# Kernel tuning notes

Hardware: AMD Instinct MI355X
Metric: run time of the kernel (lower is better)

The kernel has to match this reference:

```python
import jax, jax.numpy as jnp
import numpy as np

N, H, R2, T, E, POS, L = 50000, 256, 460, 3, 100000, 3, 2
RRELU_SLOPE = (1.0 / 8 + 1.0 / 3) / 2  # eval-mode rrelu = leaky with mean slope


def setup_inputs() -> dict:
    key = jax.random.key(0)
    ks = jax.random.split(key, 24)
    s = 0.05
    return {
        'src': jax.random.randint(ks[0], (T, E), 0, N, dtype=jnp.int32),
        'dst': jax.random.randint(ks[1], (T, E), 0, N, dtype=jnp.int32),
        'etype': jax.random.randint(ks[2], (T, E), 0, R2, dtype=jnp.int32),
        'r_to_e': jax.random.randint(ks[3], (T, E), 0, N, dtype=jnp.int32),
        'r_seg': jax.random.randint(ks[4], (T, E), 0, R2, dtype=jnp.int32),
        'pos_enc': jax.random.normal(ks[5], (T, N, POS), jnp.float32),
        'dynamic_emb': jax.random.normal(ks[6], (N, H), jnp.float32),
        'emb_rel': jax.random.normal(ks[7], (R2, H), jnp.float32) * s,
        'gru_W_ih': jax.random.normal(ks[8], (3 * H, 2 * H), jnp.float32) * s,
        'gru_W_hh': jax.random.normal(ks[9], (3 * H, H), jnp.float32) * s,
        'gru_b_ih': jnp.zeros((3 * H,), jnp.float32),
        'gru_b_hh': jnp.zeros((3 * H,), jnp.float32),
        'W_neigh': jax.random.normal(ks[10], (L, H, H), jnp.float32) * s,
        'W_loop': jax.random.normal(ks[11], (L, H, H), jnp.float32) * s,
        'W_evolve': jax.random.normal(ks[12], (L, H, H), jnp.float32) * s,
        'W_hp': jax.random.normal(ks[13], (H, H + POS), jnp.float32) * s,
        'b_hp': jnp.zeros((H,), jnp.float32),
        'W_v': jax.random.normal(ks[14], (H, H), jnp.float32) * s,
        'b_v': jnp.zeros((H,), jnp.float32),
        'W_o': jax.random.normal(ks[15], (H, H), jnp.float32) * s,
        'b_o': jnp.zeros((H,), jnp.float32),
        'time_W': jax.random.normal(ks[16], (H, H), jnp.float32) * s,
        'time_b': jnp.zeros((H,), jnp.float32),
        'glob_W': jax.random.normal(ks[17], (H, H), jnp.float32) * s,
        'glob_b': jnp.zeros((H,), jnp.float32),
    }


def _l2norm(x):
    return x / jnp.maximum(jnp.linalg.norm(x, axis=-1, keepdims=True), 1e-12)


def _gru_cell(x, hprev, W_ih, W_hh, b_ih, b_hh):
    gi = x @ W_ih.T + b_ih
    gh = hprev @ W_hh.T + b_hh
    i_r, i_z, i_n = jnp.split(gi, 3, axis=-1)
    h_r, h_z, h_n = jnp.split(gh, 3, axis=-1)
    r = jax.nn.sigmoid(i_r + h_r)
    z = jax.nn.sigmoid(i_z + h_z)
    n = jnp.tanh(i_n + r * h_n)
    return (1.0 - z) * n + z * hprev


def _forward(src, dst, etype, r_to_e, r_seg, pos_enc, dynamic_emb, emb_rel,
             gru_W_ih, gru_W_hh, gru_b_ih, gru_b_hh,
             W_neigh, W_loop, W_evolve, W_hp, b_hp, W_v, b_v, W_o, b_o,
             time_W, time_b, glob_W, glob_b):
    h = _l2norm(dynamic_emb)  # layer_norm=True path: F.normalize
    h0 = emb_rel
    outs = []
    for t in range(T):  # sequence_len snapshots
        # per-relation mean of involved entity embeddings (r_len/uniq_r spans)
        feat = h[r_to_e[t]]                                   # [E, H]
        sums = jax.ops.segment_sum(feat, r_seg[t], num_segments=R2)
        cnts = jax.ops.segment_sum(jnp.ones((E,), feat.dtype), r_seg[t], num_segments=R2)
        x_mean = jnp.where(cnts[:, None] > 0, sums / jnp.maximum(cnts, 1.0)[:, None], 0.0)
        x_in = jnp.concatenate([emb_rel, x_mean], axis=1)     # [R2, 2H]
        h0 = _l2norm(_gru_cell(x_in, h0, gru_W_ih, gru_W_hh, gru_b_ih, gru_b_hh))
        # UnionRGCN layers: msg = (h_src + rel[etype]) @ W_neigh, sum-agg * 1/in_deg,
        # plus self-loop (loop_weight if in_deg>0 else evolve_loop_weight), rrelu.
        deg = jax.ops.segment_sum(jnp.ones((E,), h.dtype), dst[t], num_segments=N)
        norm = jnp.where(deg > 0, 1.0 / jnp.maximum(deg, 1.0), 0.0)[:, None]
        nh = h
        for l in range(L):
            msg = (nh[src[t]] + h0[etype[t]]) @ W_neigh[l]    # [E, H]
            agg = jax.ops.segment_sum(msg, dst[t], num_segments=N) * norm
            loop = jnp.where(deg[:, None] > 0, nh @ W_loop[l], nh @ W_evolve[l])
            pre = agg + loop
            nh = jnp.where(pre >= 0, pre, RRELU_SLOPE * pre)
        current_h = nh
        # global attention over seq-len-1 -> out_proj(v_proj(x)) in eval mode
        atten_in = jnp.tanh(jnp.concatenate([current_h, pos_enc[t]], axis=1) @ W_hp.T + b_hp)
        global_h = (atten_in @ W_v.T + b_v) @ W_o.T + b_o
        current_h = _l2norm(current_h)
        tw = jax.nn.sigmoid(h @ time_W + time_b)
        h = tw * current_h + (1.0 - tw) * h
        gw = jax.nn.sigmoid(h @ glob_W + glob_b)
        outs.append(gw * global_h + (1.0 - gw) * h)
    return jnp.stack(outs)  # [T, N, H] history_embs


def reference(src, dst, etype, r_to_e, r_seg, pos_enc, dynamic_emb, emb_rel,
              gru_W_ih, gru_W_hh, gru_b_ih, gru_b_hh,
              W_neigh, W_loop, W_evolve, W_hp, b_hp, W_v, b_v, W_o, b_o,
              time_W, time_b, glob_W, glob_b):
    return _forward(src, dst, etype, r_to_e, r_seg, pos_enc, dynamic_emb, emb_rel,
                    gru_W_ih, gru_W_hh, gru_b_ih, gru_b_hh,
                    W_neigh, W_loop, W_evolve, W_hp, b_hp, W_v, b_v, W_o, b_o,
                    time_W, time_b, glob_W, glob_b)
```

## Files before the change

kernel.cpp:

```cpp
#include <hip/hip_runtime.h>
#include <math.h>

#define NN 50000
#define HH 256
#define RR 460
#define TT 3
#define EE 100000
#define PP 3
#define SLOPE 0.22916666666666666f
#define NBIN (RR + NN)
#define NBIN3 (3*NBIN)

typedef __bf16 bf16_t;
typedef bf16_t bf16x8 __attribute__((ext_vector_type(8)));
typedef float f32x4 __attribute__((ext_vector_type(4)));

static const size_t NHf = (size_t)NN * HH;

__device__ __forceinline__ float sigm(float x){ return 1.0f/(1.0f+__expf(-x)); }
__device__ __forceinline__ float leaky(float x){ return (x >= 0.f) ? x : SLOPE*x; }

__device__ __forceinline__ void gload_lds16(const void* g, void* l){
  __builtin_amdgcn_global_load_lds((const __attribute__((address_space(1))) void*)g,
                                   (__attribute__((address_space(3))) void*)l, 16, 0, 0);
}

__global__ __launch_bounds__(256) void tconv_all_k(
    const float* __restrict__ Wn, const float* __restrict__ Wl, const float* __restrict__ We,
    const float* __restrict__ timW, const float* __restrict__ globW,
    bf16_t* __restrict__ bst2, bf16_t* __restrict__ wdT,
    bf16_t* __restrict__ timT, bf16_t* __restrict__ globT){
  int z = blockIdx.z;
  const float* in; const float* in2 = nullptr; bf16_t* outp; int ldout;
  switch(z){
    case 0: in = Wn;           outp = bst2;                       ldout = 512; break;
    case 1: in = Wl;           outp = bst2 + 256;                 ldout = 512; break;
    case 2: in = Wn + 65536;   outp = bst2 + (size_t)256*512;     ldout = 512; break;
    case 3: in = Wl + 65536;   outp = bst2 + (size_t)256*512+256; ldout = 512; break;
    case 4: in = We;          in2 = Wl;         outp = wdT;         ldout = 256; break;
    case 5: in = We + 65536;  in2 = Wl + 65536; outp = wdT + 65536; ldout = 256; break;
    case 6: in = timW;  outp = timT;  ldout = 256; break;
    default:in = globW; outp = globT; ldout = 256; break;
  }
  __shared__ float tile[32][33];
  int n0 = blockIdx.x*32, k0 = blockIdx.y*32;
  int tx = threadIdx.x & 31, ty = threadIdx.x >> 5;
  #pragma unroll
  for (int j=0;j<4;j++){
    size_t idx = (size_t)(k0+ty+j*8)*256 + n0+tx;
    float v = in[idx];
    if (in2) v -= in2[idx];
    tile[ty+j*8][tx] = v;
  }
  __syncthreads();
  #pragma unroll
  for (int j=0;j<4;j++)
    outp[(size_t)(n0+ty+j*8)*ldout + k0+tx] = (bf16_t)tile[tx][ty+j*8];
}

__global__ __launch_bounds__(256) void copyall_k(const float* __restrict__ gW_ih,
    const float* __restrict__ gW_hh, const float* __restrict__ W_hp, const float* __restrict__ emb_rel,
    bf16_t* __restrict__ wihAT, bf16_t* __restrict__ wihBT, bf16_t* __restrict__ whhT,
    bf16_t* __restrict__ whpT, bf16_t* __restrict__ h0b){
  int r = blockIdx.x, c = threadIdx.x, y = blockIdx.y;
  if (y == 0)      wihAT[(size_t)r*256+c] = (bf16_t)gW_ih[(size_t)r*512 + c];
  else if (y == 1) wihBT[(size_t)r*256+c] = (bf16_t)gW_ih[(size_t)r*512 + 256 + c];
  else if (y == 2) whhT[(size_t)r*256+c]  = (bf16_t)gW_hh[(size_t)r*256 + c];
  else if (y == 3){ if (r < 256) whpT[(size_t)r*256+c] = (bf16_t)W_hp[(size_t)r*259 + c]; }
  else            { if (r < RR)  h0b[(size_t)r*256+c]  = (bf16_t)emb_rel[(size_t)r*256 + c]; }
}

__global__ __launch_bounds__(256) void misc_k(const float* __restrict__ W_hp, float* __restrict__ WP,
    const float* __restrict__ W_o, const float* __restrict__ b_v, const float* __restrict__ b_o,
    float* __restrict__ b_ov){
  if (blockIdx.x == 0){
    int j = threadIdx.x;
    #pragma unroll
    for (int p=0;p<PP;p++) WP[p*HH + j] = W_hp[(size_t)j*259 + HH + p];
  } else {
    int n = threadIdx.x;
    float s = b_o[n];
    for (int j=0;j<256;j++) s += W_o[(size_t)n*256+j]*b_v[j];
    b_ov[n] = s;
  }
}

__global__ __launch_bounds__(256) void copy_bfw_k(const float* __restrict__ in, bf16_t* __restrict__ outp){
  int r = blockIdx.x, c = threadIdx.x;
  outp[(size_t)r*HH + c] = (bf16_t)in[(size_t)r*HH + c];
}

__global__ __launch_bounds__(256) void sgemm_k(const float* __restrict__ A, const float* __restrict__ B,
                                               float* __restrict__ C, int M, int N, int K){
  __shared__ float As[16][128];
  __shared__ float Bs[16][64];
  int tid = threadIdx.x;
  int tx = tid & 15, ty = tid >> 4;
  int rowBase = blockIdx.x * 128;
  int colBase = blockIdx.y * 64;
  float acc[8][4];
  #pragma unroll
  for (int i=0;i<8;i++)
    #pragma unroll
    for (int j=0;j<4;j++) acc[i][j]=0.f;
  for (int k0=0;k0<K;k0+=16){
    #pragma unroll
    for (int ss=0; ss<2; ss++){
      int s = tid + ss*256;
      int r = s >> 2;
      int kk = (s & 3)*4;
      float4 v = make_float4(0.f,0.f,0.f,0.f);
      int grow = rowBase + r;
      if (grow < M) v = *(const float4*)(A + (size_t)grow*K + k0 + kk);
      As[kk+0][r]=v.x; As[kk+1][r]=v.y; As[kk+2][r]=v.z; As[kk+3][r]=v.w;
    }
    {
      int r = tid >> 4, cc = (tid & 15)*4;
      float4 v = *(const float4*)(B + (size_t)(k0+r)*N + colBase + cc);
      *(float4*)&Bs[r][cc] = v;
    }
    __syncthreads();
    #pragma unroll
    for (int kk=0;kk<16;kk++){
      float a[8], b[4];
      *(float4*)&a[0] = *(const float4*)&As[kk][ty*8];
      *(float4*)&a[4] = *(const float4*)&As[kk][ty*8+4];
      *(float4*)&b[0] = *(const float4*)&Bs[kk][tx*4];
      #pragma unroll
      for (int i=0;i<8;i++)
        #pragma unroll
        for (int j=0;j<4;j++)
          acc[i][j] = fmaf(a[i], b[j], acc[i][j]);
    }
    __syncthreads();
  }
  #pragma unroll
  for (int i=0;i<8;i++){
    int gr = rowBase + ty*8 + i;
    if (gr >= M) continue;
    float4 v = make_float4(acc[i][0], acc[i][1], acc[i][2], acc[i][3]);
    *(float4*)(C + (size_t)gr*N + colBase + tx*4) = v;
  }
}

template<int EPI, int HASB>
__global__ __launch_bounds__(256) void mgemm_k(
    const bf16_t* __restrict__ A0, const bf16_t* __restrict__ Bt,
    float* __restrict__ C, const float* __restrict__ bias,
    int M, int N, int K, const float* __restrict__ e1){
  __shared__ bf16_t As[128*64];
  __shared__ bf16_t Bs[128*64];
  int tid = threadIdx.x;
  int lane = tid & 63, w = tid >> 6;
  int wm = w >> 1, wn = w & 1;
  int rowBase = blockIdx.x * 128;
  int colBase = blockIdx.y * 128;
  f32x4 acc[4][4] = {};

  int lrow = lane >> 3;
  int p    = lane & 7;
  int arow[4];
  #pragma unroll
  for (int c = 0; c < 4; c++){
    int gr = rowBase + c*32 + w*8 + lrow;
    arow[c] = min(gr, M-1);
  }
  for (int k0 = 0; k0 < K; k0 += 64){
    #pragma unroll
    for (int c = 0; c < 4; c++){
      int r = c*32 + w*8 + lrow;
      int s = p ^ (r & 7);
      gload_lds16(A0 + (size_t)arow[c]*K + k0 + s*8, As + (size_t)(c*32 + w*8)*64);
      int gb = colBase + r;
      gload_lds16(Bt + (size_t)gb*K + k0 + s*8, Bs + (size_t)(c*32 + w*8)*64);
    }
    asm volatile("s_waitcnt vmcnt(0)" ::: "memory");
    __syncthreads();
    #pragma unroll
    for (int kk = 0; kk < 2; kk++){
      bf16x8 af[4], bfr[4];
      int sg = kk*4 + (lane >> 4);
      #pragma unroll
      for (int i = 0; i < 4; i++){
        int r = wm*64 + i*16 + (lane & 15);
        af[i] = *(const bf16x8*)(As + r*64 + (sg ^ (r & 7))*8);
      }
      #pragma unroll
      for (int j = 0; j < 4; j++){
        int rn = wn*64 + j*16 + (lane & 15);
        bfr[j] = *(const bf16x8*)(Bs + rn*64 + (sg ^ (rn & 7))*8);
      }
      #pragma unroll
      for (int i = 0; i < 4; i++)
        #pragma unroll
        for (int j = 0; j < 4; j++)
          acc[i][j] = __builtin_amdgcn_mfma_f32_16x16x32_bf16(af[i], bfr[j], acc[i][j], 0, 0, 0);
    }
    __syncthreads();
  }
  int colv[4]; float bb[4];
  #pragma unroll
  for (int j = 0; j < 4; j++){
    colv[j] = colBase + wn*64 + j*16 + (lane & 15);
    bb[j] = HASB ? bias[colv[j]] : 0.f;
  }
  #pragma unroll
  for (int i = 0; i < 4; i++){
    #pragma unroll
    for (int q = 0; q < 4; q++){
      int grt = rowBase + wm*64 + i*16 + ((lane >> 4) << 2) + q;
      if (grt >= M) continue;
      #pragma unroll
      for (int j = 0; j < 4; j++){
        size_t idx = (size_t)grt*N + colv[j];
        float v = acc[i][j][q] + bb[j];
        if (EPI == 8) v += e1[idx];
        C[idx] = v;
      }
    }
  }
}

template<int EPI, int WF32, int WBF, int HASB, int SPLITA>
__global__ __launch_bounds__(512, 6) void mgemm2_k(
    const bf16_t* __restrict__ A0, const bf16_t* __restrict__ A1,
    const bf16_t* __restrict__ Bt,
    float* __restrict__ C, bf16_t* __restrict__ Cb, const float* __restrict__ bias,
    int M, int K,
    const float* __restrict__ e1, const float* __restrict__ e2,
    const bf16_t* __restrict__ eb, const bf16_t* __restrict__ eb2,
    const int* __restrict__ degp, const int* __restrict__ z, const int* __restrict__ nzp){
  int rowBase = blockIdx.x * 64;
  int nzv = 0;
  if (EPI == 5){
    nzv = nzp[0];
    if (rowBase >= nzv) return;
  }
  __shared__ bf16_t As[64*64];
  __shared__ bf16_t Bs[256*64];
  int tid = threadIdx.x;
  int lane = tid & 63, w = tid >> 6;
  f32x4 acc[4][2] = {};

  int lrow8 = lane >> 3;
  int p     = lane & 7;
  int arow;
  {
    int r = w*8 + lrow8;
    int gr = rowBase + r;
    if (EPI == 5) arow = z[min(gr, nzv-1)];
    else          arow = min(gr, M-1);
  }
  for (int k0 = 0; k0 < K; k0 += 64){
    const bf16_t* Ap; int koff; size_t lda;
    if (SPLITA){ Ap = (k0 < 256) ? A0 : A1; koff = k0 & 255; lda = 256; }
    else       { Ap = A0; koff = k0; lda = (size_t)K; }
    {
      int r = w*8 + lrow8;
      int s = p ^ (r & 7);
      gload_lds16(Ap + (size_t)arow*lda + koff + s*8, As + (size_t)(w*8)*64);
    }
    #pragma unroll
    for (int c = 0; c < 4; c++){
      int r = w*32 + c*8 + lrow8;
      int s = p ^ (r & 7);
      gload_lds16(Bt + (size_t)r*K + k0 + s*8, Bs + (size_t)(w*32 + c*8)*64);
    }
    asm volatile("s_waitcnt vmcnt(0)" ::: "memory");
    __syncthreads();
    #pragma unroll
    for (int kk = 0; kk < 2; kk++){
      bf16x8 af[4], bfr[2];
      int sg = kk*4 + (lane >> 4);
      #pragma unroll
      for (int i = 0; i < 4; i++){
        int r = i*16 + (lane & 15);
        af[i] = *(const bf16x8*)(As + r*64 + (sg ^ (r & 7))*8);
      }
      #pragma unroll
      for (int j = 0; j < 2; j++){
        int rn = w*32 + j*16 + (lane & 15);
        bfr[j] = *(const bf16x8*)(Bs + rn*64 + (sg ^ (rn & 7))*8);
      }
      #pragma unroll
      for (int i = 0; i < 4; i++)
        #pragma unroll
        for (int j = 0; j < 2; j++)
          acc[i][j] = __builtin_amdgcn_mfma_f32_16x16x32_bf16(af[i], bfr[j], acc[i][j], 0, 0, 0);
    }
    __syncthreads();
  }
  int colv[2]; float bb[2], wp0[2], wp1[2], wp2[2];
  #pragma unroll
  for (int j = 0; j < 2; j++){
    colv[j] = w*32 + j*16 + (lane & 15);
    bb[j] = HASB ? bias[colv[j]] : 0.f;
    if (EPI == 2){ wp0[j] = e2[colv[j]]; wp1[j] = e2[256+colv[j]]; wp2[j] = e2[512+colv[j]]; }
  }
  #pragma unroll
  for (int i = 0; i < 4; i++){
    #pragma unroll
    for (int q = 0; q < 4; q++){
      int grt = rowBase + i*16 + ((lane >> 4) << 2) + q;
      if (EPI == 5){ if (grt >= nzv) continue; }
      else         { if (grt >= M) continue; }
      int orow = (EPI == 5) ? z[grt] : grt;
      int dflag = 0;
      if (EPI == 4) dflag = degp[orow];
      float p0=0.f, p1=0.f, p2=0.f;
      if (EPI == 2){ p0 = e1[(size_t)grt*3]; p1 = e1[(size_t)grt*3+1]; p2 = e1[(size_t)grt*3+2]; }
      #pragma unroll
      for (int j = 0; j < 2; j++){
        size_t idx = (size_t)orow*256 + colv[j];
        float v = acc[i][j][q] + bb[j];
        if (EPI == 2) v = tanhf(v + p0*wp0[j] + p1*wp1[j] + p2*wp2[j]);
        if (EPI == 3){
          float g = sigm(v);
          v = g*(float)eb[idx] + (1.f-g)*(float)eb2[idx];
        }
        if (EPI == 4) v = (dflag > 0) ? leaky(v) : v;
        if (EPI == 5){
          float praw = (float)Cb[idx];
          v = leaky(praw + v);
        }
        if (EPI == 7) v = sigm(v);
        if (WF32) C[idx] = v;
        if (WBF)  Cb[idx] = (bf16_t)v;
      }
    }
  }
}

__global__ __launch_bounds__(256) void l2norm_k(const float* __restrict__ in, bf16_t* __restrict__ outb){
  int i = blockIdx.x, c = threadIdx.x;
  size_t idx = (size_t)i*HH + c;
  float v = in[idx];
  float ss = v*v;
  #pragma unroll
  for (int o=32;o;o>>=1) ss += __shfl_down(ss, o);
  __shared__ float red[4];
  if ((threadIdx.x & 63)==0) red[threadIdx.x>>6] = ss;
  __syncthreads();
  float tot = red[0]+red[1]+red[2]+red[3];
  outb[idx] = (bf16_t)(v / fmaxf(sqrtf(tot), 1e-12f));
}

__global__ __launch_bounds__(256) void hist3_k(const int* __restrict__ r_seg, const int* __restrict__ dst,
                                               int* __restrict__ cnt){
  int q = blockIdx.x*256 + threadIdx.x;
  if (q >= 3*2*EE) return;
  int t = q / (2*EE);
  int e = q - t*2*EE;
  if (e < EE) atomicAdd(cnt + t*NBIN + r_seg[(size_t)t*EE + e], 1);
  else        atomicAdd(cnt + t*NBIN + RR + dst[(size_t)t*EE + (e-EE)], 1);
}

__global__ __launch_bounds__(1024) void scan1_k(const int* __restrict__ cnt, int* __restrict__ start,
                                                int* __restrict__ bsum, int n){
  __shared__ int s[1024];
  int t = blockIdx.x*1024 + threadIdx.x;
  int v = (t < n) ? cnt[t] : 0;
  s[threadIdx.x] = v;
  __syncthreads();
  for (int off = 1; off < 1024; off <<= 1){
    int x = (threadIdx.x >= off) ? s[threadIdx.x - off] : 0;
    __syncthreads();
    s[threadIdx.x] += x;
    __syncthreads();
  }
  if (t < n) start[t] = s[threadIdx.x] - v;
  if (threadIdx.x == 1023) bsum[blockIdx.x] = s[1023];
}
__global__ __launch_bounds__(256) void scan2_k(const int* __restrict__ bsum, int* __restrict__ boff,
                                               int* __restrict__ start, int nb, int n){
  __shared__ int s[256];
  int t = threadIdx.x;
  int v = (t < nb) ? bsum[t] : 0;
  s[t] = v;
  __syncthreads();
  for (int off = 1; off < 256; off <<= 1){
    int x = (t >= off) ? s[t-off] : 0;
    __syncthreads();
    s[t] += x;
    __syncthreads();
  }
  if (t < nb) boff[t] = s[t] - v;
  if (t == 255) start[n] = s[255];
}
__global__ __launch_bounds__(1024) void scan3_k(int* __restrict__ start, int* __restrict__ cur,
                                                const int* __restrict__ boff, int n){
  int t = blockIdx.x*1024 + threadIdx.x;
  if (t < n){
    int v = start[t] + boff[blockIdx.x];
    start[t] = v;
    cur[t] = v;
  }
}

__global__ __launch_bounds__(256) void fill3_k(const int* __restrict__ r_seg, const int* __restrict__ r_to_e,
    const int* __restrict__ dst, const int* __restrict__ src, const int* __restrict__ ety,
    int* __restrict__ cur, int* __restrict__ rnode, unsigned* __restrict__ dpack){
  int q = blockIdx.x*256 + threadIdx.x;
  if (q >= 3*2*EE) return;
  int t = q / (2*EE);
  int e = q - t*2*EE;
  if (e < EE){
    size_t ge = (size_t)t*EE + e;
    int pp = atomicAdd(cur + t*NBIN + r_seg[ge], 1);
    rnode[pp - EE*t] = r_to_e[ge];
  } else {
    size_t ge = (size_t)t*EE + (e - EE);
    int pp = atomicAdd(cur + t*NBIN + RR + dst[ge], 1);
    dpack[pp - EE*(t+1)] = (unsigned)src[ge] | ((unsigned)ety[ge] << 16);
  }
}

__global__ __launch_bounds__(256) void compact3_k(const int* __restrict__ cnt, int* __restrict__ zAll,
                                                  int* __restrict__ nz){
  int q = blockIdx.x*256 + threadIdx.x;
  int lane = threadIdx.x & 63;
  bool valid = q < 3*NN;
  int qc = valid ? q : 3*NN - 1;
  int t = qc / NN, d = qc - t*NN;
  bool pred = valid && (cnt[t*NBIN + RR + d] == 0);
  int tA = __shfl(t, 0), tB = __shfl(t, 63);
  if (tA == tB){
    unsigned long long m = __ballot(pred);
    int total = __popcll(m);
    int base = 0;
    if (lane == 0 && total > 0) base = atomicAdd(nz + tA, total);
    base = __shfl(base, 0);
    if (pred){
      int myoff = __popcll(m & ((1ULL << lane) - 1ULL));
      zAll[(size_t)tA*NN + base + myoff] = d;
    }
  } else {
    if (pred){
      int pp = atomicAdd(nz + t, 1);
      zAll[(size_t)t*NN + pp] = d;
    }
  }
}

__global__ __launch_bounds__(256) void rmean_k(const int* __restrict__ startT, const int* __restrict__ rnode,
    const bf16_t* __restrict__ hb, bf16_t* __restrict__ meanb, int rbase){
  int r = blockIdx.x, c = threadIdx.x;
  int s0 = startT[r] - rbase, s1 = startT[r+1] - rbase;
  float acc = 0.f, acc2 = 0.f;
  int i = s0;
  for (; i + 1 < s1; i += 2){
    acc  += (float)hb[(size_t)rnode[i]*HH + c];
    acc2 += (float)hb[(size_t)rnode[i+1]*HH + c];
  }
  if (i < s1) acc += (float)hb[(size_t)rnode[i]*HH + c];
  acc += acc2;
  int cnt = s1 - s0;
  meanb[(size_t)r*HH + c] = (bf16_t)((cnt > 0) ? acc/(float)cnt : 0.f);
}

__global__ __launch_bounds__(256) void gru_gate_k(const float* __restrict__ gi,
    const float* __restrict__ ghb, float* __restrict__ h0, bf16_t* __restrict__ h0b){
  int r = blockIdx.x, c = threadIdx.x;
  float ir = gi[(size_t)r*768 + c],       hr = ghb[(size_t)r*768 + c];
  float iz = gi[(size_t)r*768 + 256 + c], hz = ghb[(size_t)r*768 + 256 + c];
  float in_ = gi[(size_t)r*768 + 512 + c], hn = ghb[(size_t)r*768 + 512 + c];
  float rg = sigm(ir + hr);
  float z  = sigm(iz + hz);
  float n  = tanhf(in_ + rg*hn);
  float hp = h0[(size_t)r*HH + c];
  float v = (1.f - z)*n + z*hp;
  float ss = v*v;
  #pragma unroll
  for (int o=32;o;o>>=1) ss += __shfl_down(ss, o);
  __shared__ float red[4];
  if ((threadIdx.x & 63)==0) red[threadIdx.x>>6] = ss;
  __syncthreads();
  float tot = red[0]+red[1]+red[2]+red[3];
  float nv = v / fmaxf(sqrtf(tot), 1e-12f);
  h0[(size_t)r*HH + c] = nv;
  h0b[(size_t)r*HH + c] = (bf16_t)nv;
}

__global__ __launch_bounds__(256) void gatherM_k(const bf16_t* __restrict__ nin,
    const bf16_t* __restrict__ h0b, const int* __restrict__ startT,
    const unsigned* __restrict__ dpack, bf16_t* __restrict__ Amean, int ebase){
  int w = threadIdx.x >> 6, ln = threadIdx.x & 63;
  int d = blockIdx.x*4 + w;
  if (d >= NN) return;
  int s0 = startT[RR + d] - ebase, s1 = startT[RR + d + 1] - ebase;
  int deg = s1 - s0;
  float a0=0.f, a1=0.f, a2=0.f, a3=0.f;
  int i = s0;
  for (; i + 1 < s1; i += 2){
    unsigned seA = dpack[i], seB = dpack[i+1];
    uint2 raA = *(const uint2*)(nin + (size_t)(seA & 0xffffu)*HH + ln*4);
    uint2 raB = *(const uint2*)(nin + (size_t)(seB & 0xffffu)*HH + ln*4);
    uint2 rbA = *(const uint2*)(h0b + (size_t)(seA >> 16)*HH + ln*4);
    uint2 rbB = *(const uint2*)(h0b + (size_t)(seB >> 16)*HH + ln*4);
    a0 += __uint_as_float((raA.x & 0xffffu) << 16) + __uint_as_float((rbA.x & 0xffffu) << 16)
        + __uint_as_float((raB.x & 0xffffu) << 16) + __uint_as_float((rbB.x & 0xffffu) << 16);
    a1 += __uint_as_float(raA.x & 0xffff0000u)     + __uint_as_float(rbA.x & 0xffff0000u)
        + __uint_as_float(raB.x & 0xffff0000u)     + __uint_as_float(rbB.x & 0xffff0000u);
    a2 += __uint_as_float((raA.y & 0xffffu) << 16) + __uint_as_float((rbA.y & 0xffffu) << 16)
        + __uint_as_float((raB.y & 0xffffu) << 16) + __uint_as_float((rbB.y & 0xffffu) << 16);
    a3 += __uint_as_float(raA.y & 0xffff0000u)     + __uint_as_float(rbA.y & 0xffff0000u)
        + __uint_as_float(raB.y & 0xffff0000u)     + __uint_as_float(rbB.y & 0xffff0000u);
  }
  if (i < s1){
    unsigned se = dpack[i];
    uint2 ra = *(const uint2*)(nin + (size_t)(se & 0xffffu)*HH + ln*4);
    uint2 rb = *(const uint2*)(h0b + (size_t)(se >> 16)*HH + ln*4);
    a0 += __uint_as_float((ra.x & 0xffffu) << 16) + __uint_as_float((rb.x & 0xffffu) << 16);
    a1 += __uint_as_float(ra.x & 0xffff0000u)     + __uint_as_float(rb.x & 0xffff0000u);
    a2 += __uint_as_float((ra.y & 0xffffu) << 16) + __uint_as_float((rb.y & 0xffffu) << 16);
    a3 += __uint_as_float(ra.y & 0xffff0000u)     + __uint_as_float(rb.y & 0xffff0000u);
  }
  float inv = (deg > 0) ? 1.f/(float)deg : 0.f;
  bf16_t m[4] = { (bf16_t)(a0*inv), (bf16_t)(a1*inv), (bf16_t)(a2*inv), (bf16_t)(a3*inv) };
  *(uint2*)(Amean + (size_t)d*HH + ln*4) = *(const uint2*)m;
}

__global__ __launch_bounds__(256) void l2up_k(const bf16_t* __restrict__ nh2b, const bf16_t* __restrict__ sg,
    bf16_t* __restrict__ hb){
  int i = blockIdx.x, c = threadIdx.x;
  size_t idx = (size_t)i*HH + c;
  float v = (float)nh2b[idx];
  float ss = v*v;
  #pragma unroll
  for (int o=32;o;o>>=1) ss += __shfl_down(ss, o);
  __shared__ float red[4];
  if ((threadIdx.x & 63)==0) red[threadIdx.x>>6] = ss;
  __syncthreads();
  float tot = red[0]+red[1]+red[2]+red[3];
  float curn = v / fmaxf(sqrtf(tot), 1e-12f);
  float s = (float)sg[idx];
  float hn = s*curn + (1.f-s)*(float)hb[idx];
  hb[idx] = (bf16_t)hn;
}

extern "C" void kernel_launch(void* const* d_in, const int* in_sizes, int n_in,
                              void* d_out, int out_size, void* d_ws, size_t ws_size,
                              hipStream_t stream) {
  const int*   src     = (const int*)  d_in[0];
  const int*   dst     = (const int*)  d_in[1];
  const int*   etype   = (const int*)  d_in[2];
  const int*   r_to_e  = (const int*)  d_in[3];
  const int*   r_seg   = (const int*)  d_in[4];
  const float* pos_enc = (const float*)d_in[5];
  const float* dyn_emb = (const float*)d_in[6];
  const float* emb_rel = (const float*)d_in[7];
  const float* gW_ih   = (const float*)d_in[8];
  const float* gW_hh   = (const float*)d_in[9];
  const float* gb_ih   = (const float*)d_in[10];
  const float* gb_hh   = (const float*)d_in[11];
  const float* W_neigh = (const float*)d_in[12];
  const float* W_loop  = (const float*)d_in[13];
  const float* W_evolve= (const float*)d_in[14];
  const float* W_hp    = (const float*)d_in[15];
  const float* b_hp    = (const float*)d_in[16];
  const float* W_v     = (const float*)d_in[17];
  const float* b_v     = (const float*)d_in[18];
  const float* W_o     = (const float*)d_in[19];
  const float* b_o     = (const float*)d_in[20];
  const float* time_W  = (const float*)d_in[21];
  const float* time_b  = (const float*)d_in[22];
  const float* glob_W  = (const float*)d_in[23];
  const float* glob_b  = (const float*)d_in[24];
  float* out = (float*)d_out;
  (void)in_sizes; (void)n_in; (void)out_size; (void)ws_size;

  char* ws = (char*)d_ws;
  size_t off = 0;
  auto allocB = [&](size_t bytes)->char*{
    char* pp = ws + off; off += (bytes + 255) & ~(size_t)255;
    return pp;
  };
  float*  tmp    = (float*) allocB(NHf*4);
  bf16_t* h_bf   = (bf16_t*)allocB(NHf*2);
  bf16_t* nh_bf  = (bf16_t*)allocB(NHf*2);
  bf16_t* nh2_bf = (bf16_t*)allocB(NHf*2);
  bf16_t* gh_bf  = (bf16_t*)allocB(NHf*2);
  bf16_t* Amean  = (bf16_t*)tmp;
  bf16_t* sgate  = (bf16_t*)(tmp + NHf/2);
  bf16_t* attn_bf= nh_bf;

  float*  h0    = (float*) allocB((size_t)RR*HH*4);
  bf16_t* h0b   = (bf16_t*)allocB((size_t)RR*HH*2);
  bf16_t* meanb = (bf16_t*)allocB((size_t)RR*HH*2);
  float*  gi0   = (float*) allocB((size_t)RR*768*4);
  float*  gi    = (float*) allocB((size_t)RR*768*4);
  float*  ghb   = (float*) allocB((size_t)RR*768*4);
  bf16_t* wihAT = (bf16_t*)allocB((size_t)768*256*2);
  bf16_t* wihBT = (bf16_t*)allocB((size_t)768*256*2);
  bf16_t* whhT  = (bf16_t*)allocB((size_t)768*256*2);
  float*  WP    = (float*) allocB((size_t)PP*HH*4);
  float*  WovF  = (float*) allocB((size_t)HH*HH*4);
  float*  b_ov  = (float*) allocB((size_t)HH*4);
  bf16_t* bst2  = (bf16_t*)allocB((size_t)2*HH*512*2);
  bf16_t* wdT   = (bf16_t*)allocB((size_t)2*HH*HH*2);
  bf16_t* whpT  = (bf16_t*)allocB((size_t)HH*HH*2);
  bf16_t* wovT  = (bf16_t*)allocB((size_t)HH*HH*2);
  bf16_t* timT  = (bf16_t*)allocB((size_t)HH*HH*2);
  bf16_t* globT = (bf16_t*)allocB((size_t)HH*HH*2);
  int* cnt    = (int*)allocB((size_t)(NBIN3+4)*4);
  int* start  = (int*)allocB((size_t)(NBIN3+1)*4);
  int* cur    = (int*)allocB((size_t)NBIN3*4);
  int* rnode  = (int*)allocB((size_t)3*EE*4);
  unsigned* dpack = (unsigned*)allocB((size_t)3*EE*4);
  int* zAll   = (int*)allocB((size_t)3*NN*4);
  int* bsum   = (int*)allocB(256*4);
  int* boff   = (int*)allocB(256*4);
  int* nz     = cnt + NBIN3;

  const int MT2 = (NN + 63)/64;
  const int NB3 = (NBIN3 + 1023)/1024;

  copyall_k<<<dim3(768,5), 256, 0, stream>>>(gW_ih, gW_hh, W_hp, emb_rel,
                                             wihAT, wihBT, whhT, whpT, h0b);
  tconv_all_k<<<dim3(8,8,8), 256, 0, stream>>>(W_neigh, W_loop, W_evolve, time_W, glob_W,
                                               bst2, wdT, timT, globT);
  misc_k<<<2, 256, 0, stream>>>(W_hp, WP, W_o, b_v, b_o, b_ov);
  sgemm_k<<<dim3(2,4), 256, 0, stream>>>(W_o, W_v, WovF, 256, 256, 256);
  copy_bfw_k<<<HH, 256, 0, stream>>>(WovF, wovT);
  l2norm_k<<<NN, 256, 0, stream>>>(dyn_emb, h_bf);
  hipMemcpyAsync(h0, emb_rel, (size_t)RR*HH*4, hipMemcpyDeviceToDevice, stream);
  mgemm_k<0,1><<<dim3(4,6), 256, 0, stream>>>(h0b, wihAT, gi0, gb_ih, RR, 768, 256, nullptr);

  hipMemsetAsync(cnt, 0, (size_t)(NBIN3+4)*4, stream);
  hist3_k<<<(6*EE+255)/256, 256, 0, stream>>>(r_seg, dst, cnt);
  scan1_k<<<NB3, 1024, 0, stream>>>(cnt, start, bsum, NBIN3);
  scan2_k<<<1, 256, 0, stream>>>(bsum, boff, start, NB3, NBIN3);
  scan3_k<<<NB3, 1024, 0, stream>>>(start, cur, boff, NBIN3);
  fill3_k<<<(6*EE+255)/256, 256, 0, stream>>>(r_seg, r_to_e, dst, src, etype, cur, rnode, dpack);
  compact3_k<<<(3*NN+255)/256, 256, 0, stream>>>(cnt, zAll, nz);

  for (int t=0; t<TT; t++){
    const float* posT = pos_enc + (size_t)t*NN*PP;
    const int* startT = start + (size_t)t*NBIN;
    const int* degT   = cnt + (size_t)t*NBIN + RR;
    const int* zT     = zAll + (size_t)t*NN;
    const int* nzT    = nz + t;

    rmean_k<<<RR, 256, 0, stream>>>(startT, rnode, h_bf, meanb, EE*t);
    mgemm_k<8,0><<<dim3(4,6), 256, 0, stream>>>(meanb, wihBT, gi, nullptr, RR, 768, 256, gi0);
    mgemm_k<0,1><<<dim3(4,6), 256, 0, stream>>>(h0b, whhT, ghb, gb_hh, RR, 768, 256, nullptr);
    gru_gate_k<<<RR, 256, 0, stream>>>(gi, ghb, h0, h0b);

    gatherM_k<<<(NN+3)/4, 256, 0, stream>>>(h_bf, h0b, startT, dpack, Amean, EE*(t+1));
    mgemm2_k<4,0,1,0,1><<<MT2, 512, 0, stream>>>(Amean, h_bf, bst2, nullptr, nh_bf, nullptr,
        NN, 512, nullptr, nullptr, nullptr, nullptr, degT, nullptr, nullptr);
    mgemm2_k<5,0,1,0,0><<<MT2, 512, 0, stream>>>(h_bf, nullptr, wdT, nullptr, nh_bf, nullptr,
        NN, 256, nullptr, nullptr, nullptr, nullptr, nullptr, zT, nzT);

    gatherM_k<<<(NN+3)/4, 256, 0, stream>>>(nh_bf, h0b, startT, dpack, Amean, EE*(t+1));
    mgemm2_k<4,0,1,0,1><<<MT2, 512, 0, stream>>>(Amean, nh_bf, bst2 + (size_t)HH*512, nullptr, nh2_bf, nullptr,
        NN, 512, nullptr, nullptr, nullptr, nullptr, degT, nullptr, nullptr);
    mgemm2_k<5,0,1,0,0><<<MT2, 512, 0, stream>>>(nh_bf, nullptr, wdT + (size_t)HH*HH, nullptr, nh2_bf, nullptr,
        NN, 256, nullptr, nullptr, nullptr, nullptr, nullptr, zT, nzT);

    mgemm2_k<2,0,1,1,0><<<MT2, 512, 0, stream>>>(nh2_bf, nullptr, whpT, nullptr, attn_bf, b_hp,
        NN, 256, posT, WP, nullptr, nullptr, nullptr, nullptr, nullptr);
    mgemm2_k<0,0,1,1,0><<<MT2, 512, 0, stream>>>(attn_bf, nullptr, wovT, nullptr, gh_bf, b_ov,
        NN, 256, nullptr, nullptr, nullptr, nullptr, nullptr, nullptr, nullptr);

    mgemm2_k<7,0,1,1,0><<<MT2, 512, 0, stream>>>(h_bf, nullptr, timT, nullptr, sgate, time_b,
        NN, 256, nullptr, nullptr, nullptr, nullptr, nullptr, nullptr, nullptr);
    l2up_k<<<NN, 256, 0, stream>>>(nh2_bf, sgate, h_bf);
    mgemm2_k<3,1,0,1,0><<<MT2, 512, 0, stream>>>(h_bf, nullptr, globT, out + (size_t)t*NHf, nullptr, glob_b,
        NN, 256, nullptr, nullptr, gh_bf, h_bf, nullptr, nullptr, nullptr);
  }
}
```

Measured before the change: 1.329 ms.

## Fuse zero-degree evolve correction into neighbor GEMM via third K-segment

Replaces the separate sparse evolve-correction GEMM (over compacted zero-in-degree nodes) with a third 256-wide K segment in the main neighbor/loop GEMM. Rows with degree zero load their own features there, and other rows load a zero row. Leaky activation is then applied uniformly in the epilogue. This removes the compaction kernel, one GEMM launch per layer and the read-modify-write of nh_bf. In exchange every row does 768-deep K work instead of 512 plus sparse extra work.

```diff
diff --git a/kernel.cpp b/kernel.cpp
--- a/kernel.cpp
+++ b/kernel.cpp
@@ -28,17 +28,16 @@
 __global__ __launch_bounds__(256) void tconv_all_k(
     const float* __restrict__ Wn, const float* __restrict__ Wl, const float* __restrict__ We,
     const float* __restrict__ timW, const float* __restrict__ globW,
-    bf16_t* __restrict__ bst2, bf16_t* __restrict__ wdT,
-    bf16_t* __restrict__ timT, bf16_t* __restrict__ globT){
+    bf16_t* __restrict__ bst3, bf16_t* __restrict__ timT, bf16_t* __restrict__ globT){
   int z = blockIdx.z;
   const float* in; const float* in2 = nullptr; bf16_t* outp; int ldout;
   switch(z){
-    case 0: in = Wn;           outp = bst2;                       ldout = 512; break;
-    case 1: in = Wl;           outp = bst2 + 256;                 ldout = 512; break;
-    case 2: in = Wn + 65536;   outp = bst2 + (size_t)256*512;     ldout = 512; break;
-    case 3: in = Wl + 65536;   outp = bst2 + (size_t)256*512+256; ldout = 512; break;
-    case 4: in = We;          in2 = Wl;         outp = wdT;         ldout = 256; break;
-    case 5: in = We + 65536;  in2 = Wl + 65536; outp = wdT + 65536; ldout = 256; break;
+    case 0: in = Wn;          outp = bst3;                          ldout = 768; break;
+    case 1: in = Wl;          outp = bst3 + 256;                    ldout = 768; break;
+    case 2: in = We;         in2 = Wl;         outp = bst3 + 512;   ldout = 768; break;
+    case 3: in = Wn + 65536;  outp = bst3 + (size_t)256*768;        ldout = 768; break;
+    case 4: in = Wl + 65536;  outp = bst3 + (size_t)256*768 + 256;  ldout = 768; break;
+    case 5: in = We + 65536; in2 = Wl + 65536; outp = bst3 + (size_t)256*768 + 512; ldout = 768; break;
     case 6: in = timW;  outp = timT;  ldout = 256; break;
     default:in = globW; outp = globT; ldout = 256; break;
   }
@@ -229,13 +228,8 @@
     int M, int K,
     const float* __restrict__ e1, const float* __restrict__ e2,
     const bf16_t* __restrict__ eb, const bf16_t* __restrict__ eb2,
-    const int* __restrict__ degp, const int* __restrict__ z, const int* __restrict__ nzp){
+    const int* __restrict__ degp, const bf16_t* __restrict__ zrow){
   int rowBase = blockIdx.x * 64;
-  int nzv = 0;
-  if (EPI == 5){
-    nzv = nzp[0];
-    if (rowBase >= nzv) return;
-  }
   __shared__ bf16_t As[64*64];
   __shared__ bf16_t Bs[256*64];
   int tid = threadIdx.x;
@@ -245,20 +239,26 @@
   int lrow8 = lane >> 3;
   int p     = lane & 7;
   int arow;
+  const bf16_t* a2base = nullptr;
   {
     int r = w*8 + lrow8;
-    int gr = rowBase + r;
-    if (EPI == 5) arow = z[min(gr, nzv-1)];
-    else          arow = min(gr, M-1);
+    arow = min(rowBase + r, M-1);
+    if (SPLITA == 2) a2base = (degp[arow] == 0) ? (A1 + (size_t)arow*256) : zrow;
   }
   for (int k0 = 0; k0 < K; k0 += 64){
-    const bf16_t* Ap; int koff; size_t lda;
-    if (SPLITA){ Ap = (k0 < 256) ? A0 : A1; koff = k0 & 255; lda = 256; }
-    else       { Ap = A0; koff = k0; lda = (size_t)K; }
+    const bf16_t* Ap; int koff;
+    if (SPLITA == 2){
+      Ap = (k0 < 256) ? (A0 + (size_t)arow*256)
+         : (k0 < 512) ? (A1 + (size_t)arow*256)
+         : a2base;
+      koff = k0 & 255;
+    } else {
+      Ap = A0 + (size_t)arow*K; koff = k0;
+    }
     {
       int r = w*8 + lrow8;
       int s = p ^ (r & 7);
-      gload_lds16(Ap + (size_t)arow*lda + koff + s*8, As + (size_t)(w*8)*64);
+      gload_lds16(Ap + koff + s*8, As + (size_t)(w*8)*64);
     }
     #pragma unroll
     for (int c = 0; c < 4; c++){
@@ -302,27 +302,19 @@
     #pragma unroll
     for (int q = 0; q < 4; q++){
       int grt = rowBase + i*16 + ((lane >> 4) << 2) + q;
-      if (EPI == 5){ if (grt >= nzv) continue; }
-      else         { if (grt >= M) continue; }
-      int orow = (EPI == 5) ? z[grt] : grt;
-      int dflag = 0;
-      if (EPI == 4) dflag = degp[orow];
+      if (grt >= M) continue;
       float p0=0.f, p1=0.f, p2=0.f;
       if (EPI == 2){ p0 = e1[(size_t)grt*3]; p1 = e1[(size_t)grt*3+1]; p2 = e1[(size_t)grt*3+2]; }
       #pragma unroll
       for (int j = 0; j < 2; j++){
-        size_t idx = (size_t)orow*256 + colv[j];
+        size_t idx = (size_t)grt*256 + colv[j];
         float v = acc[i][j][q] + bb[j];
         if (EPI == 2) v = tanhf(v + p0*wp0[j] + p1*wp1[j] + p2*wp2[j]);
         if (EPI == 3){
           float g = sigm(v);
           v = g*(float)eb[idx] + (1.f-g)*(float)eb2[idx];
         }
-        if (EPI == 4) v = (dflag > 0) ? leaky(v) : v;
-        if (EPI == 5){
-          float praw = (float)Cb[idx];
-          v = leaky(praw + v);
-        }
+        if (EPI == 6) v = leaky(v);
         if (EPI == 7) v = sigm(v);
         if (WF32) C[idx] = v;
         if (WBF)  Cb[idx] = (bf16_t)v;
@@ -412,33 +404,6 @@
     size_t ge = (size_t)t*EE + (e - EE);
     int pp = atomicAdd(cur + t*NBIN + RR + dst[ge], 1);
     dpack[pp - EE*(t+1)] = (unsigned)src[ge] | ((unsigned)ety[ge] << 16);
-  }
-}
-
-__global__ __launch_bounds__(256) void compact3_k(const int* __restrict__ cnt, int* __restrict__ zAll,
-                                                  int* __restrict__ nz){
-  int q = blockIdx.x*256 + threadIdx.x;
-  int lane = threadIdx.x & 63;
-  bool valid = q < 3*NN;
-  int qc = valid ? q : 3*NN - 1;
-  int t = qc / NN, d = qc - t*NN;
-  bool pred = valid && (cnt[t*NBIN + RR + d] == 0);
-  int tA = __shfl(t, 0), tB = __shfl(t, 63);
-  if (tA == tB){
-    unsigned long long m = __ballot(pred);
-    int total = __popcll(m);
-    int base = 0;
-    if (lane == 0 && total > 0) base = atomicAdd(nz + tA, total);
-    base = __shfl(base, 0);
-    if (pred){
-      int myoff = __popcll(m & ((1ULL << lane) - 1ULL));
-      zAll[(size_t)tA*NN + base + myoff] = d;
-    }
-  } else {
-    if (pred){
-      int pp = atomicAdd(nz + t, 1);
-      zAll[(size_t)t*NN + pp] = d;
-    }
   }
 }
 
@@ -596,29 +561,28 @@
   float*  WP    = (float*) allocB((size_t)PP*HH*4);
   float*  WovF  = (float*) allocB((size_t)HH*HH*4);
   float*  b_ov  = (float*) allocB((size_t)HH*4);
-  bf16_t* bst2  = (bf16_t*)allocB((size_t)2*HH*512*2);
-  bf16_t* wdT   = (bf16_t*)allocB((size_t)2*HH*HH*2);
+  bf16_t* bst3  = (bf16_t*)allocB((size_t)2*HH*768*2);
   bf16_t* whpT  = (bf16_t*)allocB((size_t)HH*HH*2);
   bf16_t* wovT  = (bf16_t*)allocB((size_t)HH*HH*2);
   bf16_t* timT  = (bf16_t*)allocB((size_t)HH*HH*2);
   bf16_t* globT = (bf16_t*)allocB((size_t)HH*HH*2);
+  bf16_t* zrow  = (bf16_t*)allocB(512);
   int* cnt    = (int*)allocB((size_t)(NBIN3+4)*4);
   int* start  = (int*)allocB((size_t)(NBIN3+1)*4);
   int* cur    = (int*)allocB((size_t)NBIN3*4);
   int* rnode  = (int*)allocB((size_t)3*EE*4);
   unsigned* dpack = (unsigned*)allocB((size_t)3*EE*4);
-  int* zAll   = (int*)allocB((size_t)3*NN*4);
   int* bsum   = (int*)allocB(256*4);
   int* boff   = (int*)allocB(256*4);
-  int* nz     = cnt + NBIN3;
 
   const int MT2 = (NN + 63)/64;
   const int NB3 = (NBIN3 + 1023)/1024;
 
+  hipMemsetAsync(zrow, 0, 512, stream);
   copyall_k<<<dim3(768,5), 256, 0, stream>>>(gW_ih, gW_hh, W_hp, emb_rel,
                                              wihAT, wihBT, whhT, whpT, h0b);
   tconv_all_k<<<dim3(8,8,8), 256, 0, stream>>>(W_neigh, W_loop, W_evolve, time_W, glob_W,
-                                               bst2, wdT, timT, globT);
+                                               bst3, timT, globT);
   misc_k<<<2, 256, 0, stream>>>(W_hp, WP, W_o, b_v, b_o, b_ov);
   sgemm_k<<<dim3(2,4), 256, 0, stream>>>(W_o, W_v, WovF, 256, 256, 256);
   copy_bfw_k<<<HH, 256, 0, stream>>>(WovF, wovT);
@@ -632,14 +596,11 @@
   scan2_k<<<1, 256, 0, stream>>>(bsum, boff, start, NB3, NBIN3);
   scan3_k<<<NB3, 1024, 0, stream>>>(start, cur, boff, NBIN3);
   fill3_k<<<(6*EE+255)/256, 256, 0, stream>>>(r_seg, r_to_e, dst, src, etype, cur, rnode, dpack);
-  compact3_k<<<(3*NN+255)/256, 256, 0, stream>>>(cnt, zAll, nz);
 
   for (int t=0; t<TT; t++){
     const float* posT = pos_enc + (size_t)t*NN*PP;
     const int* startT = start + (size_t)t*NBIN;
     const int* degT   = cnt + (size_t)t*NBIN + RR;
-    const int* zT     = zAll + (size_t)t*NN;
-    const int* nzT    = nz + t;
 
     rmean_k<<<RR, 256, 0, stream>>>(startT, rnode, h_bf, meanb, EE*t);
     mgemm_k<8,0><<<dim3(4,6), 256, 0, stream>>>(meanb, wihBT, gi, nullptr, RR, 768, 256, gi0);
@@ -647,26 +608,22 @@
     gru_gate_k<<<RR, 256, 0, stream>>>(gi, ghb, h0, h0b);
 
     gatherM_k<<<(NN+3)/4, 256, 0, stream>>>(h_bf, h0b, startT, dpack, Amean, EE*(t+1));
-    mgemm2_k<4,0,1,0,1><<<MT2, 512, 0, stream>>>(Amean, h_bf, bst2, nullptr, nh_bf, nullptr,
-        NN, 512, nullptr, nullptr, nullptr, nullptr, degT, nullptr, nullptr);
-    mgemm2_k<5,0,1,0,0><<<MT2, 512, 0, stream>>>(h_bf, nullptr, wdT, nullptr, nh_bf, nullptr,
-        NN, 256, nullptr, nullptr, nullptr, nullptr, nullptr, zT, nzT);
+    mgemm2_k<6,0,1,0,2><<<MT2, 512, 0, stream>>>(Amean, h_bf, bst3, nullptr, nh_bf, nullptr,
+        NN, 768, nullptr, nullptr, nullptr, nullptr, degT, zrow);
 
     gatherM_k<<<(NN+3)/4, 256, 0, stream>>>(nh_bf, h0b, startT, dpack, Amean, EE*(t+1));
-    mgemm2_k<4,0,1,0,1><<<MT2, 512, 0, stream>>>(Amean, nh_bf, bst2 + (size_t)HH*512, nullptr, nh2_bf, nullptr,
-        NN, 512, nullptr, nullptr, nullptr, nullptr, degT, nullptr, nullptr);
-    mgemm2_k<5,0,1,0,0><<<MT2, 512, 0, stream>>>(nh_bf, nullptr, wdT + (size_t)HH*HH, nullptr, nh2_bf, nullptr,
-        NN, 256, nullptr, nullptr, nullptr, nullptr, nullptr, zT, nzT);
+    mgemm2_k<6,0,1,0,2><<<MT2, 512, 0, stream>>>(Amean, nh_bf, bst3 + (size_t)HH*768, nullptr, nh2_bf, nullptr,
+        NN, 768, nullptr, nullptr, nullptr, nullptr, degT, zrow);
 
     mgemm2_k<2,0,1,1,0><<<MT2, 512, 0, stream>>>(nh2_bf, nullptr, whpT, nullptr, attn_bf, b_hp,
-        NN, 256, posT, WP, nullptr, nullptr, nullptr, nullptr, nullptr);
+        NN, 256, posT, WP, nullptr, nullptr, nullptr, nullptr);
     mgemm2_k<0,0,1,1,0><<<MT2, 512, 0, stream>>>(attn_bf, nullptr, wovT, nullptr, gh_bf, b_ov,
-        NN, 256, nullptr, nullptr, nullptr, nullptr, nullptr, nullptr, nullptr);
+        NN, 256, nullptr, nullptr, nullptr, nullptr, nullptr, nullptr);
 
     mgemm2_k<7,0,1,1,0><<<MT2, 512, 0, stream>>>(h_bf, nullptr, timT, nullptr, sgate, time_b,
-        NN, 256, nullptr, nullptr, nullptr, nullptr, nullptr, nullptr, nullptr);
+        NN, 256, nullptr, nullptr, nullptr, nullptr, nullptr, nullptr);
     l2up_k<<<NN, 256, 0, stream>>>(nh2_bf, sgate, h_bf);
     mgemm2_k<3,1,0,1,0><<<MT2, 512, 0, stream>>>(h_bf, nullptr, globT, out + (size_t)t*NHf, nullptr, glob_b,
-        NN, 256, nullptr, nullptr, gh_bf, h_bf, nullptr, nullptr, nullptr);
-  }
-}
+        NN, 256, nullptr, nullptr, gh_bf, h_bf, nullptr, nullptr);
+  }
+}
```

Result: faster. 1.220 ms (-8.2%).
